# Optimization experiments

Hardware: AMD Instinct MI355X
Metric: run time of the kernel (lower is better)

## Reference

```python
import jax, jax.numpy as jnp
import numpy as np

HEADS = 4
HEAD_DIM = 32
SCALE = HEAD_DIM ** (-0.5)


def setup_inputs() -> dict:
    key = jax.random.key(0)
    k1, k2, k3, k4 = jax.random.split(key, 4)
    x = jax.random.normal(k1, (32, 256, 64, 64), dtype=jnp.float32)
    # to_qkv: Conv2d(256 -> 3*heads*head_dim=384, kernel 1x1, bias=False)
    w_qkv = jax.random.normal(k2, (384, 256), dtype=jnp.float32) * 0.02
    # to_out: Conv2d(128 -> 256, kernel 1x1, bias=True)
    w_out = jax.random.normal(k3, (256, 128), dtype=jnp.float32) * 0.02
    b_out = jax.random.normal(k4, (256,), dtype=jnp.float32) * 0.02
    return {"x": x, "w_qkv": w_qkv, "w_out": w_out, "b_out": b_out}


def reference(x, w_qkv, w_out, b_out):
    b, c, H, W = x.shape
    n = H * W
    # 1x1 conv == channel matmul; produce (b, 3, heads, head_dim, n)
    qkv = jnp.einsum('oc,bchw->bohw', w_qkv, x).reshape(b, 3, HEADS, HEAD_DIM, n)
    q, k, v = qkv[:, 0], qkv[:, 1], qkv[:, 2]  # each (b, h, d, n)
    q = jax.nn.softmax(q, axis=-1) * SCALE     # softmax over spatial n
    k = jax.nn.softmax(k, axis=-2)             # softmax over channel d
    # context: (b, h, e, d) -- reduce over n
    context = jnp.einsum('bhen,bhdn->bhed', k, v)
    # out: (b, h, d, n)
    out = jnp.einsum('bhed,bhen->bhdn', context, q)
    out = out.reshape(b, HEADS * HEAD_DIM, H, W)
    # to_out 1x1 conv with bias
    return jnp.einsum('oc,bchw->bohw', w_out, out) + b_out[None, :, None, None]
```

## Files before the change

kernel.cpp:

```cpp
#include <hip/hip_runtime.h>
#include <hip/hip_bf16.h>

#define NTOK 4096
#define SCALE 0.17677669529663687f

#define SWZ(r) ((((r) >> 1) ^ ((r) >> 3)) & 3)

using f32x4 = __attribute__((ext_vector_type(4))) float;
using s16x8 = __attribute__((ext_vector_type(8))) short;
using v4i   = __attribute__((ext_vector_type(4))) int;

__device__ __forceinline__ ushort bf_rne(float f) {
  unsigned int u = __builtin_bit_cast(unsigned int, f);
  u += 0x7FFFu + ((u >> 16) & 1u);
  return (ushort)(u >> 16);
}
__device__ __forceinline__ unsigned int pk2(float a, float b) {
  __hip_bfloat162 h = __float22bfloat162_rn(make_float2(a, b));
  unsigned int u;
  __builtin_memcpy(&u, &h, 4);
  return u;
}
__device__ __forceinline__ void gl_lds16(const ushort* g, ushort* l) {
  __builtin_amdgcn_global_load_lds(
      (const __attribute__((address_space(1))) unsigned int*)g,
      (__attribute__((address_space(3))) unsigned int*)l, 16, 0, 0);
}
__device__ __forceinline__ v4i make_srsrc(const void* p) {
  union {
    struct { const void* p; unsigned nr; unsigned fl; } s;
    v4i v;
  } u;
  u.s.p = p;
  u.s.nr = 0xFFFFFFFFu;
  u.s.fl = 0x00020000u;
  return u.v;
}
#if __has_builtin(__builtin_amdgcn_raw_buffer_load_f32)
#define HAVE_RAW_BL 1
#else
#define HAVE_RAW_BL 0
#endif

__global__ __launch_bounds__(256) void k_cvt_w(const float* __restrict__ w,
                                               ushort* __restrict__ wb) {
  const int i = blockIdx.x * 256 + threadIdx.x;
  const float4 v = reinterpret_cast<const float4*>(w)[i];
  ushort4 h;
  h.x = bf_rne(v.x); h.y = bf_rne(v.y); h.z = bf_rne(v.z); h.w = bf_rne(v.w);
  reinterpret_cast<ushort4*>(wb)[i] = h;
}

__global__ __launch_bounds__(256) void k_qkv_mfma(const float* __restrict__ x,
                                                  const ushort* __restrict__ wb,
                                                  ushort* __restrict__ Ecn,
                                                  ushort* __restrict__ kb,
                                                  ushort* __restrict__ vb,
                                                  float* __restrict__ spart) {
  const int n0 = blockIdx.x * 128;
  const int o0 = blockIdx.y * 128;
  const int b  = blockIdx.z;
  const float* xb = x + (size_t)b * 256 * NTOK;

  __shared__ ushort As[4096];
  __shared__ ushort Bs[4096];

  const int t = threadIdx.x;
  const int lane = t & 63;
  const int wv = t >> 6;
  const int wr = wv >> 1, wc = wv & 1;
  const int lm = lane & 15;
  const int lk = lane >> 4;

  int aoff[4], boff[4];
#pragma unroll
  for (int mf = 0; mf < 4; ++mf) {
    const int ar = wr * 64 + mf * 16 + lm;
    aoff[mf] = ar * 32 + 8 * (lk ^ SWZ(ar));
  }
#pragma unroll
  for (int nf = 0; nf < 4; ++nf) {
    const int br = wc * 64 + nf * 16 + lm;
    boff[nf] = br * 32 + 8 * (lk ^ SWZ(br));
  }
  const int s1 = t, s2 = t + 256;
  const int r1 = s1 >> 2, q1 = (s1 & 3) ^ SWZ(r1);
  const int r2 = s2 >> 2, q2 = (s2 & 3) ^ SWZ(r2);
  const size_t ga1 = (size_t)(o0 + r1) * 256 + q1 * 8;
  const size_t ga2 = (size_t)(o0 + r2) * 256 + q2 * 8;
  const int lbase1 = wv * 512;
  const int lbase2 = 2048 + wv * 512;
  int sst[2], sn[2], sco[2];
#pragma unroll
  for (int i = 0; i < 2; ++i) {
    const int u = t + 256 * i;
    sn[i] = u & 127;
    sco[i] = u >> 7;
    sst[i] = sn[i] * 32 + 8 * (sco[i] ^ SWZ(sn[i]));
  }
  const float* xbn = xb + n0;
  const v4i rx = make_srsrc(xbn);
  int voff[2];
#pragma unroll
  for (int i = 0; i < 2; ++i) voff[i] = (sco[i] * 8 * NTOK + sn[i]) * 4;

  f32x4 acc[4][4];
#pragma unroll
  for (int i = 0; i < 4; ++i)
#pragma unroll
    for (int j = 0; j < 4; ++j) acc[i][j] = (f32x4){0.f, 0.f, 0.f, 0.f};

  float pre[16];
#pragma unroll
  for (int i = 0; i < 2; ++i)
#pragma unroll
    for (int j = 0; j < 8; ++j) {
#if HAVE_RAW_BL
      pre[i * 8 + j] = __builtin_amdgcn_raw_buffer_load_f32(rx, voff[i], j * 16384, 0);
#else
      pre[i * 8 + j] = xbn[(size_t)(sco[i] * 8 + j) * NTOK + sn[i]];
#endif
    }

  for (int it = 0; it < 8; ++it) {
    const size_t c0 = (size_t)it * 32;
    gl_lds16(wb + ga1 + c0, As + lbase1);
    gl_lds16(wb + ga2 + c0, As + lbase2);
#pragma unroll
    for (int i = 0; i < 2; ++i) {
      union { s16x8 v; unsigned int u[4]; } pk;
      pk.u[0] = pk2(pre[i * 8 + 0], pre[i * 8 + 1]);
      pk.u[1] = pk2(pre[i * 8 + 2], pre[i * 8 + 3]);
      pk.u[2] = pk2(pre[i * 8 + 4], pre[i * 8 + 5]);
      pk.u[3] = pk2(pre[i * 8 + 6], pre[i * 8 + 7]);
      *reinterpret_cast<s16x8*>(Bs + sst[i]) = pk.v;
    }
    __syncthreads();
    if (it < 7) {
      const int so = (it + 1) * 524288;
#pragma unroll
      for (int i = 0; i < 2; ++i)
#pragma unroll
        for (int j = 0; j < 8; ++j) {
#if HAVE_RAW_BL
          pre[i * 8 + j] = __builtin_amdgcn_raw_buffer_load_f32(rx, voff[i], so + j * 16384, 0);
#else
          pre[i * 8 + j] = xbn[(size_t)((it + 1) * 32 + sco[i] * 8 + j) * NTOK + sn[i]];
#endif
        }
    }
    s16x8 af[4], bf[4];
#pragma unroll
    for (int mf = 0; mf < 4; ++mf)
      af[mf] = *reinterpret_cast<const s16x8*>(As + aoff[mf]);
#pragma unroll
    for (int nf = 0; nf < 4; ++nf)
      bf[nf] = *reinterpret_cast<const s16x8*>(Bs + boff[nf]);
#pragma unroll
    for (int mf = 0; mf < 4; ++mf)
#pragma unroll
      for (int nf = 0; nf < 4; ++nf)
        acc[mf][nf] = __builtin_amdgcn_mfma_f32_16x16x32_bf16(af[mf], bf[nf], acc[mf][nf], 0, 0, 0);
    __syncthreads();
  }

  if (blockIdx.y == 0) {
    ushort* C = Ecn + (size_t)b * 128 * NTOK + n0;
    float* sp = spart + (((size_t)b * 32 + blockIdx.x) * 2 + wc) * 128;
#pragma unroll
    for (int mf = 0; mf < 4; ++mf) {
#pragma unroll
      for (int r = 0; r < 4; ++r) {
        const int ch = wr * 64 + mf * 16 + lk * 4 + r;
        float s = 0.f;
#pragma unroll
        for (int nf = 0; nf < 4; ++nf) {
          const float e = __expf(acc[mf][nf][r]);
          s += e;
          C[(size_t)ch * NTOK + wc * 64 + nf * 16 + lm] = bf_rne(e);
        }
        s += __shfl_xor(s, 1, 64);
        s += __shfl_xor(s, 2, 64);
        s += __shfl_xor(s, 4, 64);
        s += __shfl_xor(s, 8, 64);
        if (lm == 0) sp[ch] = s;
      }
    }
  } else if (blockIdx.y == 1) {
#pragma unroll
    for (int nf = 0; nf < 4; ++nf) {
#pragma unroll
      for (int g = 0; g < 2; ++g) {
        float m = -1e30f;
#pragma unroll
        for (int mm = 0; mm < 2; ++mm)
#pragma unroll
          for (int r = 0; r < 4; ++r)
            m = fmaxf(m, acc[g * 2 + mm][nf][r]);
        m = fmaxf(m, __shfl_xor(m, 16, 64));
        m = fmaxf(m, __shfl_xor(m, 32, 64));
        float s = 0.f;
#pragma unroll
        for (int mm = 0; mm < 2; ++mm)
#pragma unroll
          for (int r = 0; r < 4; ++r) {
            const float e = __expf(acc[g * 2 + mm][nf][r] - m);
            acc[g * 2 + mm][nf][r] = e;
            s += e;
          }
        s += __shfl_xor(s, 16, 64);
        s += __shfl_xor(s, 32, 64);
        const float inv = 1.0f / s;
#pragma unroll
        for (int mm = 0; mm < 2; ++mm)
#pragma unroll
          for (int r = 0; r < 4; ++r) acc[g * 2 + mm][nf][r] *= inv;
      }
    }
    ushort* C = kb + (size_t)b * 128 * NTOK + n0;
#pragma unroll
    for (int mf = 0; mf < 4; ++mf) {
      const int row0 = wr * 64 + mf * 16 + lk * 4;
#pragma unroll
      for (int nf = 0; nf < 4; ++nf) {
        const int col = wc * 64 + nf * 16 + lm;
#pragma unroll
        for (int r = 0; r < 4; ++r)
          C[(size_t)(row0 + r) * NTOK + col] = bf_rne(acc[mf][nf][r]);
      }
    }
  } else {
    ushort* C = vb + (size_t)b * 128 * NTOK + n0;
#pragma unroll
    for (int mf = 0; mf < 4; ++mf) {
      const int row0 = wr * 64 + mf * 16 + lk * 4;
#pragma unroll
      for (int nf = 0; nf < 4; ++nf) {
        const int col = wc * 64 + nf * 16 + lm;
#pragma unroll
        for (int r = 0; r < 4; ++r)
          C[(size_t)(row0 + r) * NTOK + col] = bf_rne(acc[mf][nf][r]);
      }
    }
  }
}

__global__ __launch_bounds__(256) void k_context_mfma(const ushort* __restrict__ kb,
                                                      const ushort* __restrict__ vb,
                                                      float* __restrict__ ctx_part) {
  const int bh = blockIdx.x >> 1;
  const int half = blockIdx.x & 1;
  const int w = threadIdx.x >> 6;
  const int seg = half * 4 + w;
  const int lane = threadIdx.x & 63;
  const int lm = lane & 15, lk = lane >> 4;
  const ushort* kp = kb + (size_t)bh * 32 * NTOK + (size_t)seg * 512;
  const ushort* vp = vb + (size_t)bh * 32 * NTOK + (size_t)seg * 512;
  f32x4 acc[2][2];
#pragma unroll
  for (int i = 0; i < 2; ++i)
#pragma unroll
    for (int j = 0; j < 2; ++j) acc[i][j] = (f32x4){0.f, 0.f, 0.f, 0.f};
#pragma unroll 4
  for (int ks = 0; ks < 16; ++ks) {
    const int coff = ks * 32 + lk * 8;
    const s16x8 a0 = *reinterpret_cast<const s16x8*>(kp + (size_t)lm * NTOK + coff);
    const s16x8 a1 = *reinterpret_cast<const s16x8*>(kp + (size_t)(16 + lm) * NTOK + coff);
    const s16x8 b0 = *reinterpret_cast<const s16x8*>(vp + (size_t)lm * NTOK + coff);
    const s16x8 b1 = *reinterpret_cast<const s16x8*>(vp + (size_t)(16 + lm) * NTOK + coff);
    acc[0][0] = __builtin_amdgcn_mfma_f32_16x16x32_bf16(a0, b0, acc[0][0], 0, 0, 0);
    acc[0][1] = __builtin_amdgcn_mfma_f32_16x16x32_bf16(a0, b1, acc[0][1], 0, 0, 0);
    acc[1][0] = __builtin_amdgcn_mfma_f32_16x16x32_bf16(a1, b0, acc[1][0], 0, 0, 0);
    acc[1][1] = __builtin_amdgcn_mfma_f32_16x16x32_bf16(a1, b1, acc[1][1], 0, 0, 0);
  }
  float* op = ctx_part + ((size_t)bh * 8 + seg) * 1024;
#pragma unroll
  for (int et = 0; et < 2; ++et)
#pragma unroll
    for (int dt = 0; dt < 2; ++dt)
#pragma unroll
      for (int r = 0; r < 4; ++r)
        op[(et * 16 + lk * 4 + r) * 32 + dt * 16 + lm] = acc[et][dt][r];
}

__global__ __launch_bounds__(256) void k_w2(const float* __restrict__ ctx_part,
                                            const float* __restrict__ spart,
                                            const float* __restrict__ w_out,
                                            ushort* __restrict__ W2b) {
  const int b = blockIdx.x;
  const int t = threadIdx.x;
  __shared__ float ctx[4096];
  __shared__ float fbuf[128];
#pragma unroll
  for (int i = 0; i < 16; ++i) {
    const int idx = t + 256 * i;
    const int h = idx >> 10, ed = idx & 1023;
    const float* cp = ctx_part + ((size_t)((b * 4 + h) * 8)) * 1024 + ed;
    float a = 0.f;
#pragma unroll
    for (int j = 0; j < 8; ++j) a += cp[j * 1024];
    ctx[idx] = a;
  }
  if (t < 128) {
    float s = 0.f;
    for (int p = 0; p < 64; ++p) s += spart[((size_t)b * 64 + p) * 128 + t];
    fbuf[t] = SCALE / s;
  }
  __syncthreads();
  const float* wrow = w_out + (size_t)t * 128;
  ushort* wout_row = W2b + ((size_t)b * 256 + t) * 128;
  float wv[32];
  for (int h = 0; h < 4; ++h) {
#pragma unroll
    for (int d = 0; d < 32; ++d) wv[d] = wrow[h * 32 + d];
#pragma unroll 4
    for (int e = 0; e < 32; ++e) {
      float a = 0.f;
#pragma unroll
      for (int d = 0; d < 32; ++d) a += wv[d] * ctx[h * 1024 + e * 32 + d];
      wout_row[h * 32 + e] = bf_rne(a * fbuf[h * 32 + e]);
    }
  }
}

__global__ __launch_bounds__(256) void k_out_mfma(const ushort* __restrict__ Ecn,
                                                  const ushort* __restrict__ W2b,
                                                  const float* __restrict__ b_out,
                                                  float* __restrict__ out) {
  const int n0 = blockIdx.x * 128;
  const int o0 = blockIdx.y * 128;
  const int b  = blockIdx.z;
  const ushort* A  = W2b + (size_t)b * 256 * 128;
  const ushort* Bq = Ecn + (size_t)b * 128 * NTOK;

  __shared__ ushort As[8192];
  __shared__ ushort Bt[8192];

  const int t = threadIdx.x;
  const int lane = t & 63;
  const int wv = t >> 6;
  const int wr = wv >> 1, wc = wv & 1;
  const int lm = lane & 15;
  const int lk = lane >> 4;

  int aoff[4][2], boff[4][2];
#pragma unroll
  for (int mf = 0; mf < 4; ++mf) {
    const int ar = wr * 64 + mf * 16 + lm;
#pragma unroll
    for (int ks = 0; ks < 2; ++ks)
      aoff[mf][ks] = ar * 64 + 8 * ((ks * 4 + lk) ^ (ar & 7));
  }
#pragma unroll
  for (int nf = 0; nf < 4; ++nf) {
    const int br = wc * 64 + nf * 16 + lm;
#pragma unroll
    for (int ks = 0; ks < 2; ++ks)
      boff[nf][ks] = br * 64 + 8 * ((ks * 4 + lk) ^ (br & 7));
  }
  size_t gaA[4];
  int lb[4];
#pragma unroll
  for (int i = 0; i < 4; ++i) {
    const int s_total = t + 256 * i;
    const int r = s_total >> 3;
    const int q = (s_total & 7) ^ (r & 7);
    gaA[i] = (size_t)(o0 + r) * 128 + q * 8;
    lb[i] = wv * 512 + i * 2048;
  }
  int bst[8], bn[8], bcg[8];
#pragma unroll
  for (int i = 0; i < 8; ++i) {
    const int u = t + 256 * i;
    bn[i] = u & 127;
    bcg[i] = u >> 7;
    bst[i] = bn[i] * 64 + 8 * ((bcg[i] >> 1) ^ (bn[i] & 7)) + (bcg[i] & 1) * 4;
  }

  f32x4 acc[4][4];
#pragma unroll
  for (int i = 0; i < 4; ++i)
#pragma unroll
    for (int j = 0; j < 4; ++j) acc[i][j] = (f32x4){0.f, 0.f, 0.f, 0.f};

  for (int it = 0; it < 2; ++it) {
    const size_t c0 = (size_t)it * 64;
    __syncthreads();
#pragma unroll
    for (int i = 0; i < 4; ++i)
      gl_lds16(A + gaA[i] + c0, As + lb[i]);
#pragma unroll
    for (int i = 0; i < 8; ++i) {
      const ushort* gp = Bq + (c0 + bcg[i] * 4) * NTOK + n0 + bn[i];
      ushort4 hvec;
      hvec.x = gp[0];
      hvec.y = gp[NTOK];
      hvec.z = gp[2 * NTOK];
      hvec.w = gp[3 * NTOK];
      *reinterpret_cast<ushort4*>(Bt + bst[i]) = hvec;
    }
    __syncthreads();
#pragma unroll
    for (int ks = 0; ks < 2; ++ks) {
      s16x8 af[4], bf[4];
#pragma unroll
      for (int mf = 0; mf < 4; ++mf)
        af[mf] = *reinterpret_cast<const s16x8*>(As + aoff[mf][ks]);
#pragma unroll
      for (int nf = 0; nf < 4; ++nf)
        bf[nf] = *reinterpret_cast<const s16x8*>(Bt + boff[nf][ks]);
#pragma unroll
      for (int mf = 0; mf < 4; ++mf)
#pragma unroll
        for (int nf = 0; nf < 4; ++nf)
          acc[mf][nf] = __builtin_amdgcn_mfma_f32_16x16x32_bf16(af[mf], bf[nf], acc[mf][nf], 0, 0, 0);
    }
  }

  float* C = out + ((size_t)b * 256 + o0) * NTOK + n0;
#pragma unroll
  for (int mf = 0; mf < 4; ++mf) {
    const int row0 = wr * 64 + mf * 16 + lk * 4;
#pragma unroll
    for (int nf = 0; nf < 4; ++nf) {
      const int col = wc * 64 + nf * 16 + lm;
#pragma unroll
      for (int r = 0; r < 4; ++r) {
        const float bias = b_out[o0 + row0 + r];
        C[(size_t)(row0 + r) * NTOK + col] = acc[mf][nf][r] + bias;
      }
    }
  }
}

extern "C" void kernel_launch(void* const* d_in, const int* in_sizes, int n_in,
                              void* d_out, int out_size, void* d_ws, size_t ws_size,
                              hipStream_t stream) {
  const float* x     = (const float*)d_in[0];
  const float* w_qkv = (const float*)d_in[1];
  const float* w_out = (const float*)d_in[2];
  const float* b_out = (const float*)d_in[3];
  float* out = (float*)d_out;

  ushort* kb  = (ushort*)d_ws;
  ushort* vb  = kb + (size_t)16777216;
  ushort* Ecn = vb + (size_t)16777216;
  float*  ctx_part = (float*)(Ecn + (size_t)16777216);
  float*  spart    = ctx_part + 1048576;
  ushort* wb  = (ushort*)(spart + 262144);
  ushort* W2b = wb + 98304;

  k_cvt_w<<<96, 256, 0, stream>>>(w_qkv, wb);
  k_qkv_mfma<<<dim3(32, 3, 32), 256, 0, stream>>>(x, wb, Ecn, kb, vb, spart);
  k_context_mfma<<<256, 256, 0, stream>>>(kb, vb, ctx_part);
  k_w2<<<32, 256, 0, stream>>>(ctx_part, spart, w_out, W2b);
  k_out_mfma<<<dim3(32, 2, 32), 256, 0, stream>>>(Ecn, W2b, b_out, out);
}
```

Measured before the change: 171.5 us.

## Preload full weight tile into LDS and hand-schedule waits in QKV GEMM

The QKV projection kernel now loads the whole 128x256 bf16 weight slice into LDS once, with an XOR swizzle, before the K loop, instead of streaming 32-column chunks every iteration. Inside the loop, __syncthreads is replaced by explicit s_waitcnt vmcnt/lgkmcnt plus s_barrier with scheduling barriers, and the loop is fully unrolled. The aim is to stop per-iteration weight reloads and let the prefetch of x for the next step overlap the MFMAs. In exchange LDS per block grows to about 72KB, which can cut occupancy. The vmcnt(0) wait at the top of each iteration forces the x prefetch to finish before the MFMAs start.

```diff
diff --git a/kernel.cpp b/kernel.cpp
--- a/kernel.cpp
+++ b/kernel.cpp
@@ -62,7 +62,7 @@
   const int b  = blockIdx.z;
   const float* xb = x + (size_t)b * 256 * NTOK;
 
-  __shared__ ushort As[4096];
+  __shared__ ushort As[128 * 256];
   __shared__ ushort Bs[4096];
 
   const int t = threadIdx.x;
@@ -72,24 +72,16 @@
   const int lm = lane & 15;
   const int lk = lane >> 4;
 
-  int aoff[4], boff[4];
-#pragma unroll
-  for (int mf = 0; mf < 4; ++mf) {
-    const int ar = wr * 64 + mf * 16 + lm;
-    aoff[mf] = ar * 32 + 8 * (lk ^ SWZ(ar));
-  }
+  int boff[4];
 #pragma unroll
   for (int nf = 0; nf < 4; ++nf) {
     const int br = wc * 64 + nf * 16 + lm;
     boff[nf] = br * 32 + 8 * (lk ^ SWZ(br));
   }
-  const int s1 = t, s2 = t + 256;
-  const int r1 = s1 >> 2, q1 = (s1 & 3) ^ SWZ(r1);
-  const int r2 = s2 >> 2, q2 = (s2 & 3) ^ SWZ(r2);
-  const size_t ga1 = (size_t)(o0 + r1) * 256 + q1 * 8;
-  const size_t ga2 = (size_t)(o0 + r2) * 256 + q2 * 8;
-  const int lbase1 = wv * 512;
-  const int lbase2 = 2048 + wv * 512;
+  int arow[4];
+#pragma unroll
+  for (int mf = 0; mf < 4; ++mf) arow[mf] = wr * 64 + mf * 16 + lm;
+
   int sst[2], sn[2], sco[2];
 #pragma unroll
   for (int i = 0; i < 2; ++i) {
@@ -104,28 +96,42 @@
 #pragma unroll
   for (int i = 0; i < 2; ++i) voff[i] = (sco[i] * 8 * NTOK + sn[i]) * 4;
 
+#if HAVE_RAW_BL
+#define BLOAD(i, j, itc) __builtin_amdgcn_raw_buffer_load_f32(rx, voff[i], (itc) * 524288 + (j) * 16384, 0)
+#else
+#define BLOAD(i, j, itc) xbn[(size_t)((itc) * 32 + sco[i] * 8 + (j)) * NTOK + sn[i]]
+#endif
+
+  {
+#pragma unroll
+    for (int i = 0; i < 16; ++i) {
+      const int s = i * 256 + t;
+      const int row = s >> 5;
+      const int q = (s & 31) ^ (row & 31);
+      gl_lds16(wb + (size_t)(o0 + row) * 256 + q * 8,
+               As + (size_t)(i * 256 + wv * 64) * 8);
+    }
+  }
+  float pre[16];
+#pragma unroll
+  for (int i = 0; i < 2; ++i)
+#pragma unroll
+    for (int j = 0; j < 8; ++j) pre[i * 8 + j] = BLOAD(i, j, 0);
+  __syncthreads();
+
   f32x4 acc[4][4];
 #pragma unroll
   for (int i = 0; i < 4; ++i)
 #pragma unroll
     for (int j = 0; j < 4; ++j) acc[i][j] = (f32x4){0.f, 0.f, 0.f, 0.f};
 
-  float pre[16];
-#pragma unroll
-  for (int i = 0; i < 2; ++i)
-#pragma unroll
-    for (int j = 0; j < 8; ++j) {
-#if HAVE_RAW_BL
-      pre[i * 8 + j] = __builtin_amdgcn_raw_buffer_load_f32(rx, voff[i], j * 16384, 0);
-#else
-      pre[i * 8 + j] = xbn[(size_t)(sco[i] * 8 + j) * NTOK + sn[i]];
-#endif
-    }
-
+#pragma unroll
   for (int it = 0; it < 8; ++it) {
-    const size_t c0 = (size_t)it * 32;
-    gl_lds16(wb + ga1 + c0, As + lbase1);
-    gl_lds16(wb + ga2 + c0, As + lbase2);
+    if (it > 0) {
+      __builtin_amdgcn_sched_barrier(0);
+      asm volatile("s_waitcnt vmcnt(0)" ::: "memory");
+      __builtin_amdgcn_sched_barrier(0);
+    }
 #pragma unroll
     for (int i = 0; i < 2; ++i) {
       union { s16x8 v; unsigned int u[4]; } pk;
@@ -135,24 +141,23 @@
       pk.u[3] = pk2(pre[i * 8 + 6], pre[i * 8 + 7]);
       *reinterpret_cast<s16x8*>(Bs + sst[i]) = pk.v;
     }
-    __syncthreads();
     if (it < 7) {
-      const int so = (it + 1) * 524288;
 #pragma unroll
       for (int i = 0; i < 2; ++i)
 #pragma unroll
-        for (int j = 0; j < 8; ++j) {
-#if HAVE_RAW_BL
-          pre[i * 8 + j] = __builtin_amdgcn_raw_buffer_load_f32(rx, voff[i], so + j * 16384, 0);
-#else
-          pre[i * 8 + j] = xbn[(size_t)((it + 1) * 32 + sco[i] * 8 + j) * NTOK + sn[i]];
-#endif
-        }
-    }
+        for (int j = 0; j < 8; ++j) pre[i * 8 + j] = BLOAD(i, j, it + 1);
+    }
+    __builtin_amdgcn_sched_barrier(0);
+    asm volatile("s_waitcnt lgkmcnt(0)" ::: "memory");
+    __builtin_amdgcn_sched_barrier(0);
+    __builtin_amdgcn_s_barrier();
+    __builtin_amdgcn_sched_barrier(0);
     s16x8 af[4], bf[4];
 #pragma unroll
-    for (int mf = 0; mf < 4; ++mf)
-      af[mf] = *reinterpret_cast<const s16x8*>(As + aoff[mf]);
+    for (int mf = 0; mf < 4; ++mf) {
+      const int sc = (it * 4 + lk) ^ (arow[mf] & 31);
+      af[mf] = *reinterpret_cast<const s16x8*>(As + arow[mf] * 256 + 8 * sc);
+    }
 #pragma unroll
     for (int nf = 0; nf < 4; ++nf)
       bf[nf] = *reinterpret_cast<const s16x8*>(Bs + boff[nf]);
@@ -161,8 +166,11 @@
 #pragma unroll
       for (int nf = 0; nf < 4; ++nf)
         acc[mf][nf] = __builtin_amdgcn_mfma_f32_16x16x32_bf16(af[mf], bf[nf], acc[mf][nf], 0, 0, 0);
-    __syncthreads();
-  }
+    __builtin_amdgcn_sched_barrier(0);
+    __builtin_amdgcn_s_barrier();
+    __builtin_amdgcn_sched_barrier(0);
+  }
+#undef BLOAD
 
   if (blockIdx.y == 0) {
     ushort* C = Ecn + (size_t)b * 128 * NTOK + n0;
```

Measured after the change: 165.1 us. -3.7%, faster.
